# Performance work log

Measured on AMD Instinct MI355X. Metric: run time of the kernel, lower is better.

The kernel has to match this reference:

```python
import jax, jax.numpy as jnp
import numpy as np

BN_EPS = 1e-5


def _conv1x1(w, x):
    # w: [out, in], x: [B, in, N] -> [B, out, N]
    return jnp.einsum('oi,bin->bon', w, x)


def _bn_eval(x, g, b, m, v):
    # x: [B, C, N]; eval-mode BatchNorm1d with running stats
    scale = (g / jnp.sqrt(v + BN_EPS))[None, :, None]
    shift = (b - m * g / jnp.sqrt(v + BN_EPS))[None, :, None]
    return x * scale + shift


def _sa_layer(x, xyz, wqk, wv, bvv, wt, btt, g, b2, m, v):
    # offset-attention (SALayerCLS). q_conv and k_conv share weights -> q == k.
    h = x + xyz                                   # [B, C, N]
    q = _conv1x1(wqk, h)                          # [B, C//4, N]
    val = _conv1x1(wv, h) + bvv[None, :, None]    # [B, C, N]
    energy = jnp.einsum('bdn,bdm->bnm', q, q)     # [B, N, N]
    att = jax.nn.softmax(energy, axis=-1)
    # double normalization: L1-renormalize over dim=1 (rows)
    att = att / (1e-9 + att.sum(axis=1, keepdims=True))
    x_r = jnp.einsum('bcn,bnm->bcm', val, att)    # [B, C, N]
    t = _conv1x1(wt, x - x_r) + btt[None, :, None]
    t = jax.nn.relu(_bn_eval(t, g, b2, m, v))
    return x + t


def setup_inputs() -> dict:
    key = jax.random.key(0)
    ks = jax.random.split(key, 17)
    B, C, N = 8, 256, 2048
    f = jnp.float32
    return {
        'x': jax.random.normal(ks[0], (B, C, N), f),
        'xyz': jax.random.normal(ks[1], (B, N, 3), f),
        'conv1_w': jax.random.normal(ks[2], (C, C), f) * 0.05,
        'convpos_w': jax.random.normal(ks[3], (C, 3), f) * 0.05,
        'bn1_g': jax.random.uniform(ks[4], (C,), f, 0.5, 1.5),
        'bn1_b': jax.random.normal(ks[5], (C,), f) * 0.05,
        'bn1_m': jax.random.normal(ks[6], (C,), f) * 0.05,
        'bn1_v': jax.random.uniform(ks[7], (C,), f, 0.5, 1.5),
        'Wqk': jax.random.normal(ks[8], (4, C // 4, C), f) * 0.05,
        'Wv': jax.random.normal(ks[9], (4, C, C), f) * 0.05,
        'bv': jax.random.normal(ks[10], (4, C), f) * 0.05,
        'Wt': jax.random.normal(ks[11], (4, C, C), f) * 0.05,
        'bt': jax.random.normal(ks[12], (4, C), f) * 0.05,
        'bn_g': jax.random.uniform(ks[13], (4, C), f, 0.5, 1.5),
        'bn_b': jax.random.normal(ks[14], (4, C), f) * 0.05,
        'bn_m': jax.random.normal(ks[15], (4, C), f) * 0.05,
        'bn_v': jax.random.uniform(ks[16], (4, C), f, 0.5, 1.5),
    }


def reference(x, xyz, conv1_w, convpos_w, bn1_g, bn1_b, bn1_m, bn1_v,
              Wqk, Wv, bv, Wt, bt, bn_g, bn_b, bn_m, bn_v):
    # xyz: [B, N, 3] -> conv_pos -> [B, C, N]
    pos = jnp.einsum('oi,bni->bon', convpos_w, xyz)
    h = jax.nn.relu(_bn_eval(_conv1x1(conv1_w, x), bn1_g, bn1_b, bn1_m, bn1_v))
    outs = []
    for i in range(4):  # four stacked SA layers (structurally distinct params)
        h = _sa_layer(h, pos, Wqk[i], Wv[i], bv[i], Wt[i], bt[i],
                      bn_g[i], bn_b[i], bn_m[i], bn_v[i])
        outs.append(h)
    return jnp.concatenate(outs, axis=1)  # [B, 4*C, N]
```

## Files before the change

kernel.cpp:

```cpp
#include <hip/hip_runtime.h>
#include <hip/hip_bf16.h>
#include <math.h>

#define B_DIM 8
#define C_DIM 256
#define N_DIM 2048
#define CQ 64

#define TM 64
#define TN 64
#define TK 16

#define PV_BN 64
#define PV_BK 64

using short8 = __attribute__((ext_vector_type(8))) short;
using f32x4 = __attribute__((ext_vector_type(4))) float;

__device__ __forceinline__ unsigned short f2bf(float x) {
  union { float f; unsigned int u; } c; c.f = x;
  unsigned int r = c.u + 0x7fffu + ((c.u >> 16) & 1u);
  return (unsigned short)(r >> 16);
}
__device__ __forceinline__ float bf2f(unsigned short u) {
  union { unsigned int ui; float f; } c; c.ui = ((unsigned int)u) << 16;
  return c.f;
}

__global__ void split_kernel(const float* __restrict__ src, unsigned short* __restrict__ hi,
                             unsigned short* __restrict__ lo, int count) {
  int i = blockIdx.x * 256 + threadIdx.x;
  if (i < count) {
    float v = src[i];
    unsigned short h = f2bf(v);
    hi[i] = h;
    lo[i] = f2bf(v - bf2f(h));
  }
}

__global__ void pos_kernel(const float* __restrict__ w, const float* __restrict__ xyz,
                           float* __restrict__ pos) {
  int n = blockIdx.x * blockDim.x + threadIdx.x;
  int c = blockIdx.y;
  int b = blockIdx.z;
  const float* xp = xyz + ((long long)b * N_DIM + n) * 3;
  pos[((long long)b * C_DIM + c) * N_DIM + n] =
      w[c * 3 + 0] * xp[0] + w[c * 3 + 1] * xp[1] + w[c * 3 + 2] * xp[2];
}

__global__ void gemm_wx(const float* __restrict__ W,
                        const float* __restrict__ X, long long sxB,
                        const float* __restrict__ Xadd, long long saB,
                        const float* __restrict__ bias,
                        const float* __restrict__ bng, const float* __restrict__ bnb,
                        const float* __restrict__ bnm, const float* __restrict__ bnv,
                        const float* __restrict__ Res, long long srB,
                        float* __restrict__ Y, unsigned short* __restrict__ Ybf,
                        long long syB, int M, int K) {
  const int N = N_DIM;
  int b = blockIdx.z;
  int m0 = blockIdx.y * TM;
  int n0 = blockIdx.x * TN;
  int t = threadIdx.x;
  int tx = t & 15, ty = t >> 4;
  __shared__ float As[TK][TM + 1];
  __shared__ float Bs[TK][TN];
  float acc[4][4] = {};
  const float* Xb = X + (long long)b * sxB;
  const float* Ab = Xadd ? Xadd + (long long)b * saB : nullptr;
  for (int k0 = 0; k0 < K; k0 += TK) {
#pragma unroll
    for (int v = 0; v < 4; v++) {
      int l = t * 4 + v;
      int i = l >> 4, k = l & 15;
      As[k][i] = W[(long long)(m0 + i) * K + k0 + k];
    }
#pragma unroll
    for (int v = 0; v < 4; v++) {
      int l = t * 4 + v;
      int k = l >> 6, j = l & 63;
      float x = Xb[(long long)(k0 + k) * N + n0 + j];
      if (Ab) x += Ab[(long long)(k0 + k) * N + n0 + j];
      Bs[k][j] = x;
    }
    __syncthreads();
#pragma unroll
    for (int k = 0; k < TK; k++) {
      float a[4], bb[4];
#pragma unroll
      for (int ii = 0; ii < 4; ii++) a[ii] = As[k][ty * 4 + ii];
#pragma unroll
      for (int jj = 0; jj < 4; jj++) bb[jj] = Bs[k][tx * 4 + jj];
#pragma unroll
      for (int ii = 0; ii < 4; ii++)
#pragma unroll
        for (int jj = 0; jj < 4; jj++)
          acc[ii][jj] = fmaf(a[ii], bb[jj], acc[ii][jj]);
    }
    __syncthreads();
  }
#pragma unroll
  for (int ii = 0; ii < 4; ii++) {
    int m = m0 + ty * 4 + ii;
    float sh = bias ? bias[m] : 0.f;
    bool dobn = (bng != nullptr);
    float bnsc = 0.f, bnsh = 0.f;
    if (dobn) {
      bnsc = bng[m] * rsqrtf(bnv[m] + 1e-5f);
      bnsh = bnb[m] - bnm[m] * bnsc;
    }
#pragma unroll
    for (int jj = 0; jj < 4; jj++) {
      int n = n0 + tx * 4 + jj;
      float v = acc[ii][jj] + sh;
      if (dobn) v = fmaxf(v * bnsc + bnsh, 0.f);
      if (Res) v += Res[(long long)b * srB + (long long)m * N + n];
      if (Ybf)
        Ybf[(long long)b * syB + (long long)m * N + n] = f2bf(v);
      else
        Y[(long long)b * syB + (long long)m * N + n] = v;
    }
  }
}

__global__ __launch_bounds__(256) void gemm_mfma(
    const unsigned short* __restrict__ Whi, const unsigned short* __restrict__ Wlo,
    const float* __restrict__ X, long long sxB,
    const float* __restrict__ Xadd, long long saB,
    const float* __restrict__ bias,
    const float* __restrict__ bng, const float* __restrict__ bnb,
    const float* __restrict__ bnm, const float* __restrict__ bnv,
    const float* __restrict__ Res, long long srB,
    float* __restrict__ Y, unsigned short* __restrict__ Ybf, long long syB) {
  const int N = N_DIM, K = C_DIM;
  int b = blockIdx.z;
  int m0 = blockIdx.y * 128;
  int n0 = blockIdx.x * 64;
  int t = threadIdx.x;
  int w = t >> 6, l = t & 63;
  int lr = l & 15, lk = l >> 4;
  int j = t & 63, dq = t >> 6;
  int ar = t >> 3, as_ = t & 7;

  __shared__ __align__(16) char Ah[128 * 128];
  __shared__ __align__(16) char Al[128 * 128];
  __shared__ __align__(16) char Bh[64 * 128];
  __shared__ __align__(16) char Bl[64 * 128];

  const float* Xb = X + (long long)b * sxB;
  const float* Adb = Xadd ? Xadd + (long long)b * saB : nullptr;

  f32x4 acc[2][4];
#pragma unroll
  for (int i = 0; i < 2; i++)
#pragma unroll
    for (int jq = 0; jq < 4; jq++) acc[i][jq] = f32x4{0.f, 0.f, 0.f, 0.f};

  for (int k0 = 0; k0 < K; k0 += 64) {
    short8 wh[4], wl[4];
#pragma unroll
    for (int it = 0; it < 4; it++) {
      int r = it * 32 + ar;
      wh[it] = *(const short8*)(Whi + (long long)(m0 + r) * K + k0 + as_ * 8);
      wl[it] = *(const short8*)(Wlo + (long long)(m0 + r) * K + k0 + as_ * 8);
    }
    float v[16];
#pragma unroll
    for (int i = 0; i < 16; i++) {
      float x = Xb[(long long)(k0 + dq * 16 + i) * N + n0 + j];
      if (Adb) x += Adb[(long long)(k0 + dq * 16 + i) * N + n0 + j];
      v[i] = x;
    }
    unsigned int ph[8], pl[8];
#pragma unroll
    for (int i = 0; i < 8; i++) {
      unsigned short h0 = f2bf(v[2 * i]), h1 = f2bf(v[2 * i + 1]);
      unsigned short l0 = f2bf(v[2 * i] - bf2f(h0)), l1 = f2bf(v[2 * i + 1] - bf2f(h1));
      ph[i] = (unsigned int)h0 | ((unsigned int)h1 << 16);
      pl[i] = (unsigned int)l0 | ((unsigned int)l1 << 16);
    }
#pragma unroll
    for (int it = 0; it < 4; it++) {
      int r = it * 32 + ar;
      *(short8*)(Ah + r * 128 + ((as_ ^ (r & 7)) << 4)) = wh[it];
      *(short8*)(Al + r * 128 + ((as_ ^ (r & 7)) << 4)) = wl[it];
    }
    {
      int o0 = dq * 2, o1 = dq * 2 + 1;
      *(uint4*)(Bh + j * 128 + ((o0 ^ (j & 7)) << 4)) = make_uint4(ph[0], ph[1], ph[2], ph[3]);
      *(uint4*)(Bh + j * 128 + ((o1 ^ (j & 7)) << 4)) = make_uint4(ph[4], ph[5], ph[6], ph[7]);
      *(uint4*)(Bl + j * 128 + ((o0 ^ (j & 7)) << 4)) = make_uint4(pl[0], pl[1], pl[2], pl[3]);
      *(uint4*)(Bl + j * 128 + ((o1 ^ (j & 7)) << 4)) = make_uint4(pl[4], pl[5], pl[6], pl[7]);
    }
    __syncthreads();
#pragma unroll
    for (int sub = 0; sub < 2; sub++) {
      short8 ah[2], al2[2], bh[4], bl[4];
#pragma unroll
      for (int mi = 0; mi < 2; mi++) {
        int ra = w * 32 + mi * 16 + lr;
        ah[mi] = *(const short8*)(Ah + ra * 128 + (((sub * 4 + lk) ^ (ra & 7)) << 4));
        al2[mi] = *(const short8*)(Al + ra * 128 + (((sub * 4 + lk) ^ (ra & 7)) << 4));
      }
#pragma unroll
      for (int ni = 0; ni < 4; ni++) {
        int rb = ni * 16 + lr;
        bh[ni] = *(const short8*)(Bh + rb * 128 + (((sub * 4 + lk) ^ (rb & 7)) << 4));
        bl[ni] = *(const short8*)(Bl + rb * 128 + (((sub * 4 + lk) ^ (rb & 7)) << 4));
      }
#pragma unroll
      for (int mi = 0; mi < 2; mi++)
#pragma unroll
        for (int ni = 0; ni < 4; ni++) {
          acc[mi][ni] = __builtin_amdgcn_mfma_f32_16x16x32_bf16(ah[mi], bh[ni], acc[mi][ni], 0, 0, 0);
          acc[mi][ni] = __builtin_amdgcn_mfma_f32_16x16x32_bf16(ah[mi], bl[ni], acc[mi][ni], 0, 0, 0);
          acc[mi][ni] = __builtin_amdgcn_mfma_f32_16x16x32_bf16(al2[mi], bh[ni], acc[mi][ni], 0, 0, 0);
        }
    }
    __syncthreads();
  }
#pragma unroll
  for (int mi = 0; mi < 2; mi++) {
#pragma unroll
    for (int jj = 0; jj < 4; jj++) {
      int m = m0 + w * 32 + mi * 16 + lk * 4 + jj;
      float sh = bias ? bias[m] : 0.f;
      bool dobn = (bng != nullptr);
      float bnsc = 0.f, bnsh = 0.f;
      if (dobn) {
        bnsc = bng[m] * rsqrtf(bnv[m] + 1e-5f);
        bnsh = bnb[m] - bnm[m] * bnsc;
      }
#pragma unroll
      for (int ni = 0; ni < 4; ni++) {
        int n = n0 + ni * 16 + lr;
        float vv = acc[mi][ni][jj] + sh;
        if (dobn) vv = fmaxf(vv * bnsc + bnsh, 0.f);
        if (Res) vv += Res[(long long)b * srB + (long long)m * N + n];
        if (Ybf)
          Ybf[(long long)b * syB + (long long)m * N + n] = f2bf(vv);
        else
          Y[(long long)b * syB + (long long)m * N + n] = vv;
      }
    }
  }
}

__global__ __launch_bounds__(256) void energy_mfma(const float* __restrict__ q,
                                                   float* __restrict__ E) {
  const int N = N_DIM;
  int b = blockIdx.z;
  int r0 = blockIdx.y * 64;
  int c0 = blockIdx.x * 64;
  int t = threadIdx.x;
  int w = t >> 6, l = t & 63;
  int lr = l & 15, lk = l >> 4;
  int j = t & 63, dq = t >> 6;

  __shared__ __align__(16) char Ah[64 * 128];
  __shared__ __align__(16) char Al[64 * 128];
  __shared__ __align__(16) char Bh[64 * 128];
  __shared__ __align__(16) char Bl[64 * 128];

  const float* qb = q + (long long)b * CQ * N;
  {
    float va[16], vb[16];
#pragma unroll
    for (int i = 0; i < 16; i++) {
      va[i] = qb[(long long)(dq * 16 + i) * N + r0 + j];
      vb[i] = qb[(long long)(dq * 16 + i) * N + c0 + j];
    }
    unsigned int pah[8], pal[8], pbh[8], pbl[8];
#pragma unroll
    for (int i = 0; i < 8; i++) {
      unsigned short h0 = f2bf(va[2 * i]), h1 = f2bf(va[2 * i + 1]);
      unsigned short l0 = f2bf(va[2 * i] - bf2f(h0)), l1 = f2bf(va[2 * i + 1] - bf2f(h1));
      pah[i] = (unsigned int)h0 | ((unsigned int)h1 << 16);
      pal[i] = (unsigned int)l0 | ((unsigned int)l1 << 16);
      unsigned short g0 = f2bf(vb[2 * i]), g1 = f2bf(vb[2 * i + 1]);
      unsigned short m0_ = f2bf(vb[2 * i] - bf2f(g0)), m1 = f2bf(vb[2 * i + 1] - bf2f(g1));
      pbh[i] = (unsigned int)g0 | ((unsigned int)g1 << 16);
      pbl[i] = (unsigned int)m0_ | ((unsigned int)m1 << 16);
    }
    int o0 = dq * 2, o1 = dq * 2 + 1;
    *(uint4*)(Ah + j * 128 + ((o0 ^ (j & 7)) << 4)) = make_uint4(pah[0], pah[1], pah[2], pah[3]);
    *(uint4*)(Ah + j * 128 + ((o1 ^ (j & 7)) << 4)) = make_uint4(pah[4], pah[5], pah[6], pah[7]);
    *(uint4*)(Al + j * 128 + ((o0 ^ (j & 7)) << 4)) = make_uint4(pal[0], pal[1], pal[2], pal[3]);
    *(uint4*)(Al + j * 128 + ((o1 ^ (j & 7)) << 4)) = make_uint4(pal[4], pal[5], pal[6], pal[7]);
    *(uint4*)(Bh + j * 128 + ((o0 ^ (j & 7)) << 4)) = make_uint4(pbh[0], pbh[1], pbh[2], pbh[3]);
    *(uint4*)(Bh + j * 128 + ((o1 ^ (j & 7)) << 4)) = make_uint4(pbh[4], pbh[5], pbh[6], pbh[7]);
    *(uint4*)(Bl + j * 128 + ((o0 ^ (j & 7)) << 4)) = make_uint4(pbl[0], pbl[1], pbl[2], pbl[3]);
    *(uint4*)(Bl + j * 128 + ((o1 ^ (j & 7)) << 4)) = make_uint4(pbl[4], pbl[5], pbl[6], pbl[7]);
  }
  __syncthreads();

  f32x4 acc[4];
#pragma unroll
  for (int i = 0; i < 4; i++) acc[i] = f32x4{0.f, 0.f, 0.f, 0.f};
#pragma unroll
  for (int sub = 0; sub < 2; sub++) {
    int ra = w * 16 + lr;
    short8 ah = *(const short8*)(Ah + ra * 128 + (((sub * 4 + lk) ^ (ra & 7)) << 4));
    short8 al = *(const short8*)(Al + ra * 128 + (((sub * 4 + lk) ^ (ra & 7)) << 4));
    short8 bh[4], bl[4];
#pragma unroll
    for (int ni = 0; ni < 4; ni++) {
      int rb = ni * 16 + lr;
      bh[ni] = *(const short8*)(Bh + rb * 128 + (((sub * 4 + lk) ^ (rb & 7)) << 4));
      bl[ni] = *(const short8*)(Bl + rb * 128 + (((sub * 4 + lk) ^ (rb & 7)) << 4));
    }
#pragma unroll
    for (int ni = 0; ni < 4; ni++) {
      acc[ni] = __builtin_amdgcn_mfma_f32_16x16x32_bf16(ah, bh[ni], acc[ni], 0, 0, 0);
      acc[ni] = __builtin_amdgcn_mfma_f32_16x16x32_bf16(ah, bl[ni], acc[ni], 0, 0, 0);
      acc[ni] = __builtin_amdgcn_mfma_f32_16x16x32_bf16(al, bh[ni], acc[ni], 0, 0, 0);
    }
  }
  long long base = (long long)b * N * N;
#pragma unroll
  for (int ni = 0; ni < 4; ni++)
#pragma unroll
    for (int jj = 0; jj < 4; jj++)
      E[base + (long long)(r0 + w * 16 + lk * 4 + jj) * N + c0 + ni * 16 + lr] = acc[ni][jj];
}

__global__ void rowstats_kernel(const float* __restrict__ E, float* __restrict__ rmax,
                                float* __restrict__ rinv) {
  const int N = N_DIM;
  long long row = blockIdx.x;
  const float* p = E + row * N;
  int t = threadIdx.x;
  float v[8];
#pragma unroll
  for (int i = 0; i < 8; i++) v[i] = p[t + i * 256];
  float m = v[0];
#pragma unroll
  for (int i = 1; i < 8; i++) m = fmaxf(m, v[i]);
  for (int o = 32; o > 0; o >>= 1) m = fmaxf(m, __shfl_down(m, o, 64));
  __shared__ float red[4];
  int wid = t >> 6, lane = t & 63;
  if (lane == 0) red[wid] = m;
  __syncthreads();
  m = fmaxf(fmaxf(red[0], red[1]), fmaxf(red[2], red[3]));
  __syncthreads();
  float s = 0.f;
#pragma unroll
  for (int i = 0; i < 8; i++) s += __expf(v[i] - m);
  for (int o = 32; o > 0; o >>= 1) s += __shfl_down(s, o, 64);
  if (lane == 0) red[wid] = s;
  __syncthreads();
  if (t == 0) {
    float st = red[0] + red[1] + red[2] + red[3];
    rmax[row] = m;
    rinv[row] = 1.0f / st;
  }
}

__global__ __launch_bounds__(256, 1) void pv_mfma(
    const unsigned short* __restrict__ valbf,
    const float* __restrict__ E,
    const float* __restrict__ rmax, const float* __restrict__ rinv,
    const float* __restrict__ Hprev, long long shB, float* __restrict__ D) {
  const int N = N_DIM;
  int b = blockIdx.z;
  int n0 = blockIdx.x * PV_BN;
  int t = threadIdx.x;
  int w = t >> 6, l = t & 63;
  int lr = l & 15, lk = l >> 4;
  int brow = t >> 2, bkq = t & 3;
  int ar = t >> 3, as_ = t & 7;

  __shared__ __align__(16) char As[C_DIM * PV_BK * 2];
  __shared__ __align__(16) char Bs[PV_BN * PV_BK * 2];
  __shared__ float csred[4][PV_BN];
  __shared__ float csfin[PV_BN];

  const unsigned short* vb = valbf + (long long)b * C_DIM * N;
  const float* Ebr = E + ((long long)b * N + n0 + brow) * N;
  const float* rm = rmax + (long long)b * N;
  const float* ri = rinv + (long long)b * N;

  f32x4 acc[4][4];
#pragma unroll
  for (int i = 0; i < 4; i++)
#pragma unroll
    for (int jq = 0; jq < 4; jq++) acc[i][jq] = f32x4{0.f, 0.f, 0.f, 0.f};
  float cs = 0.f;

  float4 ev[4], rv[4], iv[4];
#pragma unroll
  for (int it = 0; it < 4; it++) {
    int kl = bkq * 4 + it * 16;
    ev[it] = *(const float4*)(Ebr + kl);
    rv[it] = *(const float4*)(rm + kl);
    iv[it] = *(const float4*)(ri + kl);
  }

  for (int k0 = 0; k0 < N; k0 += PV_BK) {
    short8 areg[8];
#pragma unroll
    for (int it = 0; it < 8; it++) {
      int r = it * 32 + ar;
      areg[it] = *(const short8*)(vb + (long long)r * N + k0 + as_ * 8);
    }
#pragma unroll
    for (int it = 0; it < 4; it++) {
      int kl = bkq * 4 + it * 16;
      float a0 = __expf(ev[it].x - rv[it].x) * iv[it].x;
      float a1 = __expf(ev[it].y - rv[it].y) * iv[it].y;
      float a2 = __expf(ev[it].z - rv[it].z) * iv[it].z;
      float a3 = __expf(ev[it].w - rv[it].w) * iv[it].w;
      unsigned short u0 = f2bf(a0), u1 = f2bf(a1), u2 = f2bf(a2), u3 = f2bf(a3);
      cs += bf2f(u0) + bf2f(u1) + bf2f(u2) + bf2f(u3);
      uint2 pk;
      pk.x = (unsigned int)u0 | ((unsigned int)u1 << 16);
      pk.y = (unsigned int)u2 | ((unsigned int)u3 << 16);
      *(uint2*)(Bs + brow * 128 + ((((kl >> 3) ^ (brow & 7)) << 4) | ((kl & 7) * 2))) = pk;
    }
#pragma unroll
    for (int it = 0; it < 8; it++) {
      int r = it * 32 + ar;
      *(short8*)(As + r * 128 + ((as_ ^ (r & 7)) << 4)) = areg[it];
    }
    __syncthreads();
    if (k0 + PV_BK < N) {
      int kb = k0 + PV_BK;
#pragma unroll
      for (int it = 0; it < 4; it++) {
        int kl = bkq * 4 + it * 16;
        ev[it] = *(const float4*)(Ebr + kb + kl);
        rv[it] = *(const float4*)(rm + kb + kl);
        iv[it] = *(const float4*)(ri + kb + kl);
      }
    }
#pragma unroll
    for (int sub = 0; sub < 2; sub++) {
      short8 af[4], bq[4];
#pragma unroll
      for (int ni = 0; ni < 4; ni++) {
        int r = ni * 16 + lr;
        bq[ni] = *(const short8*)(Bs + r * 128 + (((sub * 4 + lk) ^ (r & 7)) << 4));
      }
#pragma unroll
      for (int mi = 0; mi < 4; mi++) {
        int r = w * 64 + mi * 16 + lr;
        af[mi] = *(const short8*)(As + r * 128 + (((sub * 4 + lk) ^ (r & 7)) << 4));
      }
#pragma unroll
      for (int mi = 0; mi < 4; mi++)
#pragma unroll
        for (int ni = 0; ni < 4; ni++)
          acc[mi][ni] =
              __builtin_amdgcn_mfma_f32_16x16x32_bf16(af[mi], bq[ni], acc[mi][ni], 0, 0, 0);
    }
    __syncthreads();
  }

  csred[bkq][brow] = cs;
  __syncthreads();
  if (t < PV_BN) csfin[t] = csred[0][t] + csred[1][t] + csred[2][t] + csred[3][t];
  __syncthreads();

  const float* Hb = Hprev + (long long)b * shB;
  float* Db = D + (long long)b * C_DIM * N;
#pragma unroll
  for (int mi = 0; mi < 4; mi++) {
#pragma unroll
    for (int ni = 0; ni < 4; ni++) {
#pragma unroll
      for (int jj = 0; jj < 4; jj++) {
        int cr = w * 64 + mi * 16 + lk * 4 + jj;
        int ml = ni * 16 + lr;
        float denom = 1e-9f + csfin[ml];
        float xr = acc[mi][ni][jj] / denom;
        Db[(long long)cr * N + n0 + ml] = Hb[(long long)cr * N + n0 + ml] - xr;
      }
    }
  }
}

extern "C" void kernel_launch(void* const* d_in, const int* in_sizes, int n_in,
                              void* d_out, int out_size, void* d_ws, size_t ws_size,
                              hipStream_t stream) {
  const float* x = (const float*)d_in[0];
  const float* xyz = (const float*)d_in[1];
  const float* conv1_w = (const float*)d_in[2];
  const float* convpos_w = (const float*)d_in[3];
  const float* bn1_g = (const float*)d_in[4];
  const float* bn1_b = (const float*)d_in[5];
  const float* bn1_m = (const float*)d_in[6];
  const float* bn1_v = (const float*)d_in[7];
  const float* Wqk = (const float*)d_in[8];
  const float* Wv = (const float*)d_in[9];
  const float* bv = (const float*)d_in[10];
  const float* Wt = (const float*)d_in[11];
  const float* bt = (const float*)d_in[12];
  const float* bng = (const float*)d_in[13];
  const float* bnb = (const float*)d_in[14];
  const float* bnm = (const float*)d_in[15];
  const float* bnv = (const float*)d_in[16];
  float* out = (float*)d_out;

  const long long BCN = (long long)B_DIM * C_DIM * N_DIM;
  const long long CN = (long long)C_DIM * N_DIM;
  const long long BN = (long long)B_DIM * N_DIM;
  const int WSZ = C_DIM * C_DIM;
  float* ws = (float*)d_ws;
  float* pos = ws;
  float* h0 = pos + BCN;
  float* qbuf = h0 + BCN;
  float* dbuf = qbuf + (long long)B_DIM * CQ * N_DIM;
  float* rmax = dbuf + BCN;
  float* rinv = rmax + BN;
  unsigned short* valbf = (unsigned short*)(rinv + BN);
  unsigned short* whi = valbf + BCN;
  unsigned short* wlo = whi + 9 * WSZ;
  float* E = (float*)(wlo + 9 * WSZ);

  unsigned short* c1hi = whi;
  unsigned short* c1lo = wlo;
  unsigned short* wvhi = whi + WSZ;
  unsigned short* wvlo = wlo + WSZ;
  unsigned short* wthi = whi + 5 * WSZ;
  unsigned short* wtlo = wlo + 5 * WSZ;

  dim3 blk(256);

  split_kernel<<<dim3(WSZ / 256), blk, 0, stream>>>(conv1_w, c1hi, c1lo, WSZ);
  split_kernel<<<dim3(4 * WSZ / 256), blk, 0, stream>>>(Wv, wvhi, wvlo, 4 * WSZ);
  split_kernel<<<dim3(4 * WSZ / 256), blk, 0, stream>>>(Wt, wthi, wtlo, 4 * WSZ);

  pos_kernel<<<dim3(N_DIM / 256, C_DIM, B_DIM), blk, 0, stream>>>(convpos_w, xyz, pos);

  gemm_mfma<<<dim3(N_DIM / 64, 2, B_DIM), blk, 0, stream>>>(
      c1hi, c1lo, x, CN, nullptr, 0, nullptr,
      bn1_g, bn1_b, bn1_m, bn1_v, nullptr, 0, h0, nullptr, CN);

  for (int i = 0; i < 4; i++) {
    const float* hp = (i == 0) ? h0 : out + (long long)(i - 1) * CN;
    long long shp = (i == 0) ? CN : 4 * CN;

    gemm_wx<<<dim3(N_DIM / TN, CQ / TM, B_DIM), blk, 0, stream>>>(
        Wqk + (long long)i * CQ * C_DIM, hp, shp, pos, CN, nullptr,
        nullptr, nullptr, nullptr, nullptr, nullptr, 0,
        qbuf, nullptr, (long long)CQ * N_DIM, CQ, C_DIM);

    gemm_mfma<<<dim3(N_DIM / 64, 2, B_DIM), blk, 0, stream>>>(
        wvhi + (long long)i * WSZ, wvlo + (long long)i * WSZ, hp, shp, pos, CN,
        bv + i * C_DIM, nullptr, nullptr, nullptr, nullptr, nullptr, 0,
        nullptr, valbf, CN);

    energy_mfma<<<dim3(N_DIM / 64, N_DIM / 64, B_DIM), blk, 0, stream>>>(qbuf, E);

    rowstats_kernel<<<dim3(B_DIM * N_DIM), blk, 0, stream>>>(E, rmax, rinv);

    pv_mfma<<<dim3(N_DIM / PV_BN, 1, B_DIM), blk, 0, stream>>>(
        valbf, E, rmax, rinv, hp, shp, dbuf);

    gemm_mfma<<<dim3(N_DIM / 64, 2, B_DIM), blk, 0, stream>>>(
        wthi + (long long)i * WSZ, wtlo + (long long)i * WSZ, dbuf, CN, nullptr, 0,
        bt + i * C_DIM, bng + i * C_DIM, bnb + i * C_DIM, bnm + i * C_DIM, bnv + i * C_DIM,
        hp, shp, out + (long long)i * CN, nullptr, 4 * CN);
  }
}
```

Measured before the change: 872.0 us.

## Fuse partial softmax row stats into energy kernel and halve PV tile width

The energy kernel now computes per-64-column partial row max and exp-sum from its accumulators and writes them to a small buffer. A new light reduction kernel merges these partials, so the separate pass that re-read the full N×N energy matrix to get row statistics is gone. Separately, the PV kernel's column tile shrinks from 64 to 32 and its launch-bounds occupancy hint is removed, doubling the grid to fill more CUs. In exchange, A-operand reuse per block drops, so value traffic rises, and the energy kernel carries extra epilogue shuffles.

```diff
diff --git a/kernel.cpp b/kernel.cpp
--- a/kernel.cpp
+++ b/kernel.cpp
@@ -11,7 +11,7 @@
 #define TN 64
 #define TK 16
 
-#define PV_BN 64
+#define PV_BN 32
 #define PV_BK 64
 
 using short8 = __attribute__((ext_vector_type(8))) short;
@@ -247,7 +247,8 @@
 }
 
 __global__ __launch_bounds__(256) void energy_mfma(const float* __restrict__ q,
-                                                   float* __restrict__ E) {
+                                                   float* __restrict__ E,
+                                                   float2* __restrict__ Epart) {
   const int N = N_DIM;
   int b = blockIdx.z;
   int r0 = blockIdx.y * 64;
@@ -322,41 +323,54 @@
 #pragma unroll
     for (int jj = 0; jj < 4; jj++)
       E[base + (long long)(r0 + w * 16 + lk * 4 + jj) * N + c0 + ni * 16 + lr] = acc[ni][jj];
-}
-
-__global__ void rowstats_kernel(const float* __restrict__ E, float* __restrict__ rmax,
-                                float* __restrict__ rinv) {
-  const int N = N_DIM;
-  long long row = blockIdx.x;
-  const float* p = E + row * N;
-  int t = threadIdx.x;
-  float v[8];
-#pragma unroll
-  for (int i = 0; i < 8; i++) v[i] = p[t + i * 256];
-  float m = v[0];
-#pragma unroll
-  for (int i = 1; i < 8; i++) m = fmaxf(m, v[i]);
-  for (int o = 32; o > 0; o >>= 1) m = fmaxf(m, __shfl_down(m, o, 64));
-  __shared__ float red[4];
-  int wid = t >> 6, lane = t & 63;
-  if (lane == 0) red[wid] = m;
+
+  const long long BNr = (long long)B_DIM * N_DIM;
+#pragma unroll
+  for (int jj = 0; jj < 4; jj++) {
+    float m = fmaxf(fmaxf(acc[0][jj], acc[1][jj]), fmaxf(acc[2][jj], acc[3][jj]));
+#pragma unroll
+    for (int msk = 1; msk < 16; msk <<= 1) m = fmaxf(m, __shfl_xor(m, msk, 64));
+    float s = 0.f;
+#pragma unroll
+    for (int ni = 0; ni < 4; ni++) s += __expf(acc[ni][jj] - m);
+#pragma unroll
+    for (int msk = 1; msk < 16; msk <<= 1) s += __shfl_xor(s, msk, 64);
+    if (lr == 0) {
+      long long row = (long long)b * N + r0 + w * 16 + lk * 4 + jj;
+      Epart[(long long)(c0 >> 6) * BNr + row] = make_float2(m, s);
+    }
+  }
+}
+
+__global__ void rowstats2(const float2* __restrict__ Epart, float* __restrict__ rmax,
+                          float* __restrict__ rinv) {
+  const long long BNr = (long long)B_DIM * N_DIM;
+  int rloc = threadIdx.x & 63, qd = threadIdx.x >> 6;
+  long long row = (long long)blockIdx.x * 64 + rloc;
+  float2 v[8];
+  float m = -3.4e38f;
+#pragma unroll
+  for (int i = 0; i < 8; i++) {
+    v[i] = Epart[(long long)(qd * 8 + i) * BNr + row];
+    m = fmaxf(m, v[i].x);
+  }
+  float s = 0.f;
+#pragma unroll
+  for (int i = 0; i < 8; i++) s += v[i].y * __expf(v[i].x - m);
+  __shared__ float sm[4][64], ss[4][64];
+  sm[qd][rloc] = m;
+  ss[qd][rloc] = s;
   __syncthreads();
-  m = fmaxf(fmaxf(red[0], red[1]), fmaxf(red[2], red[3]));
-  __syncthreads();
-  float s = 0.f;
-#pragma unroll
-  for (int i = 0; i < 8; i++) s += __expf(v[i] - m);
-  for (int o = 32; o > 0; o >>= 1) s += __shfl_down(s, o, 64);
-  if (lane == 0) red[wid] = s;
-  __syncthreads();
-  if (t == 0) {
-    float st = red[0] + red[1] + red[2] + red[3];
-    rmax[row] = m;
-    rinv[row] = 1.0f / st;
-  }
-}
-
-__global__ __launch_bounds__(256, 1) void pv_mfma(
+  if (qd == 0) {
+    float M = fmaxf(fmaxf(sm[0][rloc], sm[1][rloc]), fmaxf(sm[2][rloc], sm[3][rloc]));
+    float S = ss[0][rloc] * __expf(sm[0][rloc] - M) + ss[1][rloc] * __expf(sm[1][rloc] - M) +
+              ss[2][rloc] * __expf(sm[2][rloc] - M) + ss[3][rloc] * __expf(sm[3][rloc] - M);
+    rmax[row] = M;
+    rinv[row] = 1.0f / S;
+  }
+}
+
+__global__ __launch_bounds__(256) void pv_mfma(
     const unsigned short* __restrict__ valbf,
     const float* __restrict__ E,
     const float* __restrict__ rmax, const float* __restrict__ rinv,
@@ -367,12 +381,12 @@
   int t = threadIdx.x;
   int w = t >> 6, l = t & 63;
   int lr = l & 15, lk = l >> 4;
-  int brow = t >> 2, bkq = t & 3;
+  int brow = t >> 3, bkq = t & 7;
   int ar = t >> 3, as_ = t & 7;
 
   __shared__ __align__(16) char As[C_DIM * PV_BK * 2];
   __shared__ __align__(16) char Bs[PV_BN * PV_BK * 2];
-  __shared__ float csred[4][PV_BN];
+  __shared__ float csred[8][PV_BN];
   __shared__ float csfin[PV_BN];
 
   const unsigned short* vb = valbf + (long long)b * C_DIM * N;
@@ -380,17 +394,17 @@
   const float* rm = rmax + (long long)b * N;
   const float* ri = rinv + (long long)b * N;
 
-  f32x4 acc[4][4];
+  f32x4 acc[4][2];
 #pragma unroll
   for (int i = 0; i < 4; i++)
 #pragma unroll
-    for (int jq = 0; jq < 4; jq++) acc[i][jq] = f32x4{0.f, 0.f, 0.f, 0.f};
+    for (int jq = 0; jq < 2; jq++) acc[i][jq] = f32x4{0.f, 0.f, 0.f, 0.f};
   float cs = 0.f;
 
-  float4 ev[4], rv[4], iv[4];
-#pragma unroll
-  for (int it = 0; it < 4; it++) {
-    int kl = bkq * 4 + it * 16;
+  float4 ev[2], rv[2], iv[2];
+#pragma unroll
+  for (int it = 0; it < 2; it++) {
+    int kl = bkq * 4 + it * 32;
     ev[it] = *(const float4*)(Ebr + kl);
     rv[it] = *(const float4*)(rm + kl);
     iv[it] = *(const float4*)(ri + kl);
@@ -404,8 +418,8 @@
       areg[it] = *(const short8*)(vb + (long long)r * N + k0 + as_ * 8);
     }
 #pragma unroll
-    for (int it = 0; it < 4; it++) {
-      int kl = bkq * 4 + it * 16;
+    for (int it = 0; it < 2; it++) {
+      int kl = bkq * 4 + it * 32;
       float a0 = __expf(ev[it].x - rv[it].x) * iv[it].x;
       float a1 = __expf(ev[it].y - rv[it].y) * iv[it].y;
       float a2 = __expf(ev[it].z - rv[it].z) * iv[it].z;
@@ -426,8 +440,8 @@
     if (k0 + PV_BK < N) {
       int kb = k0 + PV_BK;
 #pragma unroll
-      for (int it = 0; it < 4; it++) {
-        int kl = bkq * 4 + it * 16;
+      for (int it = 0; it < 2; it++) {
+        int kl = bkq * 4 + it * 32;
         ev[it] = *(const float4*)(Ebr + kb + kl);
         rv[it] = *(const float4*)(rm + kb + kl);
         iv[it] = *(const float4*)(ri + kb + kl);
@@ -435,9 +449,9 @@
     }
 #pragma unroll
     for (int sub = 0; sub < 2; sub++) {
-      short8 af[4], bq[4];
-#pragma unroll
-      for (int ni = 0; ni < 4; ni++) {
+      short8 af[4], bq[2];
+#pragma unroll
+      for (int ni = 0; ni < 2; ni++) {
         int r = ni * 16 + lr;
         bq[ni] = *(const short8*)(Bs + r * 128 + (((sub * 4 + lk) ^ (r & 7)) << 4));
       }
@@ -449,7 +463,7 @@
 #pragma unroll
       for (int mi = 0; mi < 4; mi++)
 #pragma unroll
-        for (int ni = 0; ni < 4; ni++)
+        for (int ni = 0; ni < 2; ni++)
           acc[mi][ni] =
               __builtin_amdgcn_mfma_f32_16x16x32_bf16(af[mi], bq[ni], acc[mi][ni], 0, 0, 0);
     }
@@ -458,7 +472,12 @@
 
   csred[bkq][brow] = cs;
   __syncthreads();
-  if (t < PV_BN) csfin[t] = csred[0][t] + csred[1][t] + csred[2][t] + csred[3][t];
+  if (t < PV_BN) {
+    float s = 0.f;
+#pragma unroll
+    for (int i = 0; i < 8; i++) s += csred[i][t];
+    csfin[t] = s;
+  }
   __syncthreads();
 
   const float* Hb = Hprev + (long long)b * shB;
@@ -466,7 +485,7 @@
 #pragma unroll
   for (int mi = 0; mi < 4; mi++) {
 #pragma unroll
-    for (int ni = 0; ni < 4; ni++) {
+    for (int ni = 0; ni < 2; ni++) {
 #pragma unroll
       for (int jj = 0; jj < 4; jj++) {
         int cr = w * 64 + mi * 16 + lk * 4 + jj;
@@ -515,7 +534,8 @@
   unsigned short* valbf = (unsigned short*)(rinv + BN);
   unsigned short* whi = valbf + BCN;
   unsigned short* wlo = whi + 9 * WSZ;
-  float* E = (float*)(wlo + 9 * WSZ);
+  float2* Epart = (float2*)(wlo + 9 * WSZ);
+  float* E = (float*)(Epart + 32 * BN);
 
   unsigned short* c1hi = whi;
   unsigned short* c1lo = wlo;
@@ -550,9 +570,9 @@
         bv + i * C_DIM, nullptr, nullptr, nullptr, nullptr, nullptr, 0,
         nullptr, valbf, CN);
 
-    energy_mfma<<<dim3(N_DIM / 64, N_DIM / 64, B_DIM), blk, 0, stream>>>(qbuf, E);
-
-    rowstats_kernel<<<dim3(B_DIM * N_DIM), blk, 0, stream>>>(E, rmax, rinv);
+    energy_mfma<<<dim3(N_DIM / 64, N_DIM / 64, B_DIM), blk, 0, stream>>>(qbuf, E, Epart);
+
+    rowstats2<<<dim3(B_DIM * N_DIM / 64), blk, 0, stream>>>(Epart, rmax, rinv);
 
     pv_mfma<<<dim3(N_DIM / PV_BN, 1, B_DIM), blk, 0, stream>>>(
         valbf, E, rmax, rinv, hp, shp, dbuf);
```

Result: faster. 826.8 us (-5.2%).
